# Performance work log

Hardware: AMD Instinct MI355X
Metric: run time of the kernel (lower is better)

The kernel has to match this reference:

```python
import jax, jax.numpy as jnp
import numpy as np

LOG_2PI = float(np.log(2.0 * np.pi))


def gaussian_log_density(samples, mean, log_squared_scale):
    inv_sigma = jnp.exp(-log_squared_scale)
    tmp = samples - mean
    return -0.5 * (tmp * tmp * inv_sigma + log_squared_scale + LOG_2PI)


def setup_inputs() -> dict:
    key = jax.random.key(0)
    k1, k2, k3, k4, k5 = jax.random.split(key, 5)
    B, L, D = 4096, 16, 512
    return {
        "data": jax.random.normal(k1, (B, D), dtype=jnp.float32),
        "reconstruction": jax.random.normal(k2, (B, D), dtype=jnp.float32),
        "z": jax.random.normal(k3, (B, L), dtype=jnp.float32),
        "z_mean": jax.random.normal(k4, (B, L), dtype=jnp.float32),
        "z_log_var": jax.random.normal(k5, (B, L), dtype=jnp.float32),
    }


def reference(data, reconstruction, z, z_mean, z_log_var):
    # reconstruction loss: mean over batch of per-sample MAE (mean over feature axis)
    recon_loss = jnp.mean(jnp.abs(data - reconstruction))

    # KL penalty: mean over batch of 0.5 * sum over latents
    summand = jnp.square(z_mean) + jnp.exp(z_log_var) - z_log_var - 1.0
    kl_loss = jnp.mean(0.5 * jnp.sum(summand, axis=1))

    # total correlation: pairwise gaussian log-density [B, B, L]
    log_qz_prob = gaussian_log_density(
        z[:, None, :], z_mean[None, :, :], z_log_var[None, :, :]
    )
    # log prod_l q(z_l): logsumexp over batch axis 1 per latent, then sum over latents
    log_qz_product = jnp.sum(jax.nn.logsumexp(log_qz_prob, axis=1), axis=1)
    # log q(z): sum over latents first, then logsumexp over batch axis
    log_qz = jax.nn.logsumexp(jnp.sum(log_qz_prob, axis=2), axis=1)
    tc_loss = jnp.mean(log_qz - log_qz_product)

    total_loss = recon_loss + kl_loss + tc_loss
    return total_loss
```

## Files before the change

kernel.cpp:

```cpp
#include <hip/hip_runtime.h>
#include <hip/hip_fp16.h>
#include <math.h>

#define BB 4096
#define LL 16
#define DD 512

#define NPTS   1024
#define XMIN   -6.0f
#define XRANGE 12.0f

#define LOG2E_F  1.4426950408889634f
#define LN2_F    0.6931471805599453f
#define LOG2PI_F 1.8378770664093453f

#define OFFC     22.942540f
#define SCALE23  8388608.0f
#define BIASF    126.94269504f

#if __has_builtin(__builtin_amdgcn_exp2f)
#define EXP2(x) __builtin_amdgcn_exp2f(x)
#else
#define EXP2(x) exp2f(x)
#endif
#if __has_builtin(__builtin_amdgcn_logf)
#define LOG2(x) __builtin_amdgcn_logf(x)
#else
#define LOG2(x) log2f(x)
#endif

typedef float f32x2 __attribute__((ext_vector_type(2)));

#define CJ_F   0
#define CT_F   147456
#define RP_F   344064
#define KLP_F  346112
#define TP_F   346368
#define TAB_F  870656
#define JP_F   887040

__device__ __forceinline__ float block_reduce(float v) {
  __shared__ float sm[4];
  __syncthreads();
#pragma unroll
  for (int off = 32; off; off >>= 1) v += __shfl_xor(v, off);
  if ((threadIdx.x & 63) == 0) sm[threadIdx.x >> 6] = v;
  __syncthreads();
  if (threadIdx.x == 0) v = (sm[0] + sm[1]) + (sm[2] + sm[3]);
  return v;
}

__global__ __launch_bounds__(256) void prep_recon_kernel(
    const float4* __restrict__ data4, const float4* __restrict__ recon4,
    const float* __restrict__ zm, const float* __restrict__ zlv,
    float* __restrict__ cj, float* __restrict__ ct,
    float* __restrict__ rp, float* __restrict__ klp,
    float* __restrict__ out) {
  const int tid = threadIdx.x;
  const int b = blockIdx.x;

  if (b == 1024 && tid == 0) out[0] = 0.0f;

  {
    const int n4 = (BB * DD) / 4;
    int stride = gridDim.x * 256;
    float s = 0.0f;
    for (int k = b * 256 + tid; k < n4; k += stride) {
      float4 a = data4[k];
      float4 r = recon4[k];
      s += (fabsf(a.x - r.x) + fabsf(a.y - r.y)) +
           (fabsf(a.z - r.z) + fabsf(a.w - r.w));
    }
    float t = block_reduce(s);
    if (tid == 0) rp[b] = t * (1.0f / (float)(BB * DD));
  }

  if (b < 256) {
    const float S = 1024.0f / 65535.0f;
    int idx = b * 256 + tid;
    int j = idx >> 4;
    int l = idx & 15;
    float m = zm[idx];
    float lv = zlv[idx];
    float inv = EXP2(-lv * LOG2E_F);
    float a = -0.5f * LOG2E_F * inv;
    float c2 = -0.5f * LOG2E_F * (lv + LOG2PI_F);
    float braw = -2.0f * a * m;
    float craw = fmaf(a, m * m, c2);

    cj[j * 36 + l]      = a * S;
    cj[j * 36 + 16 + l] = braw * S;
    float cs = (craw + OFFC) * S;
    cs += __shfl_xor(cs, 1); cs += __shfl_xor(cs, 2);
    cs += __shfl_xor(cs, 4); cs += __shfl_xor(cs, 8);
    if (l == 0) cj[j * 36 + 32] = cs;

    ct[(0 * 16 + l) * 4096 + j] = a;
    ct[(1 * 16 + l) * 4096 + j] = braw;
    ct[(2 * 16 + l) * 4096 + j] = craw;

    float kls = m * m + EXP2(lv * LOG2E_F) - lv - 1.0f;
    float s = block_reduce(kls);
    if (tid == 0) klp[b] = s * (0.5f / (float)BB);
  }
}

__global__ __launch_bounds__(256) void table_build(
    const float* __restrict__ ct, float* __restrict__ tpart) {
  __shared__ float la[128], lb[128], lc[128];
  const int tid = threadIdx.x;
  const int jc = blockIdx.x;
  const int l  = blockIdx.y;
  const int j0 = jc * 128;
  if (tid < 128) {
    la[tid] = ct[(0 * 16 + l) * 4096 + j0 + tid];
    lb[tid] = ct[(1 * 16 + l) * 4096 + j0 + tid];
    lc[tid] = ct[(2 * 16 + l) * 4096 + j0 + tid];
  }
  const float H = XRANGE / (float)(NPTS - 1);
  float x[4], acc[4];
#pragma unroll
  for (int k = 0; k < 4; ++k) {
    x[k] = XMIN + (float)(k * 256 + tid) * H;
    acc[k] = 0.0f;
  }
  __syncthreads();
#pragma unroll 2
  for (int j = 0; j < 128; ++j) {
    float a = la[j], b = lb[j], c = lc[j];
#pragma unroll
    for (int k = 0; k < 4; ++k) {
      float lp = fmaf(fmaf(a, x[k], b), x[k], c);
      acc[k] += EXP2(lp);
    }
  }
  float* o = tpart + ((size_t)jc * 16 + l) * NPTS;
#pragma unroll
  for (int k = 0; k < 4; ++k) o[k * 256 + tid] = acc[k];
}

__global__ __launch_bounds__(256) void table_reduce(
    const float* __restrict__ tpart, float* __restrict__ table) {
  const int e = blockIdx.x * 256 + threadIdx.x;
  float s = 0.0f;
#pragma unroll 4
  for (int jc = 0; jc < 32; ++jc) s += tpart[(size_t)jc * (16 * NPTS) + e];
  table[e] = s;
}

template <int CHUNK, int R>
__global__ __launch_bounds__(256, 2) void tc_joint(
    const float* __restrict__ z, const float* __restrict__ cj,
    float* __restrict__ jp) {
  __shared__ float lcj[CHUNK * 36];
  const int tid = threadIdx.x;
  const int i0 = blockIdx.x * (256 * R) + tid;
  const int j0 = blockIdx.y * CHUNK;
  const float JMUL = 65535.0f * 8192.0f;
  const float JK   = -SCALE23 * (16.0f * OFFC - BIASF);

  {
    const float4* g4 = (const float4*)(cj + (size_t)j0 * 36);
    float4* l4 = (float4*)lcj;
    for (int t = tid; t < (CHUNK * 36) / 4; t += 256) l4[t] = g4[t];
  }

  f32x2 zv[R][8];
#pragma unroll
  for (int r = 0; r < R; ++r) {
    const float4* zp = (const float4*)(z + (size_t)(i0 + 256 * r) * 16);
#pragma unroll
    for (int q = 0; q < 4; ++q) {
      float4 v = zp[q];
      zv[r][2 * q]     = (f32x2){v.x, v.y};
      zv[r][2 * q + 1] = (f32x2){v.z, v.w};
    }
  }
#pragma unroll
  for (int r = 0; r < R; ++r)
#pragma unroll
    for (int p = 0; p < 8; ++p) asm volatile("" : "+v"(zv[r][p]));

  float accJ[R];
#pragma unroll
  for (int r = 0; r < R; ++r) accJ[r] = 0.0f;

  __syncthreads();

#pragma unroll 2
  for (int j = 0; j < CHUNK; ++j) {
    const float* cp = lcj + j * 36;
    f32x2 A[8], Bv[8];
#pragma unroll
    for (int t = 0; t < 4; ++t) {
      *(float4*)&A[2 * t]  = *(const float4*)(cp + 4 * t);
      *(float4*)&Bv[2 * t] = *(const float4*)(cp + 16 + 4 * t);
    }
    float Cs = cp[32];
#pragma unroll
    for (int r = 0; r < R; ++r) {
      f32x2 acc = (f32x2){0.0f, 0.0f};
#pragma unroll
      for (int p = 0; p < 8; ++p) {
        f32x2 t2;
        asm("v_pk_fma_f32 %0, %1, %2, %3"
            : "=v"(t2) : "v"(A[p]), "v"(zv[r][p]), "v"(Bv[p]));
        asm("v_pk_fma_f32 %0, %1, %2, %0"
            : "+v"(acc) : "v"(t2), "v"(zv[r][p]));
      }
      float js = (acc.x + acc.y) + Cs;
      float w = fmaf(js, JMUL, JK);
      unsigned u;
      asm("v_cvt_u32_f32 %0, %1" : "=v"(u) : "v"(w));
      accJ[r] += __uint_as_float(u);
    }
  }

#pragma unroll
  for (int r = 0; r < R; ++r)
    jp[(size_t)blockIdx.y * BB + (size_t)(i0 + 256 * r)] = accJ[r];
}

__global__ __launch_bounds__(256) void final_kernel(
    const float* __restrict__ z, const float* __restrict__ jp,
    const float* __restrict__ table, const float* __restrict__ rp,
    const float* __restrict__ klp, float* __restrict__ out, int nc) {
  __shared__ float ltab[16 * NPTS];
  const int tid = threadIdx.x;
  const int i = blockIdx.x * 256 + tid;

  for (int t = tid; t < 16 * NPTS; t += 256) ltab[t] = table[t];

  float s0 = 0.0f, s1 = 0.0f, s2 = 0.0f, s3 = 0.0f;
  for (int c = 0; c < nc; c += 4) {
    s0 += jp[(size_t)(c + 0) * BB + i];
    s1 += jp[(size_t)(c + 1) * BB + i];
    s2 += jp[(size_t)(c + 2) * BB + i];
    s3 += jp[(size_t)(c + 3) * BB + i];
  }
  float lg = LOG2((s0 + s1) + (s2 + s3));

  __syncthreads();

  const float4* zp = (const float4*)(z + (size_t)i * 16);
  const float SC = (float)(NPTS - 1) / XRANGE;
#pragma unroll
  for (int q = 0; q < 4; ++q) {
    float4 v = zp[q];
    float xs[4] = {v.x, v.y, v.z, v.w};
#pragma unroll
    for (int k = 0; k < 4; ++k) {
      int l = 4 * q + k;
      float t = (xs[k] - XMIN) * SC;
      t = fminf(fmaxf(t, 0.0f), (float)(NPTS - 2) + 0.999f);
      int g = (int)t;
      float f = t - (float)g;
      float m0 = ltab[l * NPTS + g];
      float m1 = ltab[l * NPTS + g + 1];
      lg -= LOG2(fmaf(f, m1 - m0, m0));
    }
  }

  float tval = lg * (LN2_F / (float)BB);
  if (blockIdx.x == 0) {
#pragma unroll
    for (int q = 0; q < 8; ++q) tval += rp[tid + 256 * q];
    tval += klp[tid];
  }

  __syncthreads();
#pragma unroll
  for (int off = 32; off; off >>= 1) tval += __shfl_xor(tval, off);
  if ((tid & 63) == 0) ltab[tid >> 6] = tval;
  __syncthreads();
  if (tid == 0) atomicAdd(out, (ltab[0] + ltab[1]) + (ltab[2] + ltab[3]));
}

extern "C" void kernel_launch(void* const* d_in, const int* in_sizes, int n_in,
                              void* d_out, int out_size, void* d_ws, size_t ws_size,
                              hipStream_t stream) {
  const float* data  = (const float*)d_in[0];
  const float* recon = (const float*)d_in[1];
  const float* z     = (const float*)d_in[2];
  const float* zm    = (const float*)d_in[3];
  const float* zlv   = (const float*)d_in[4];
  float* out = (float*)d_out;
  float* ws  = (float*)d_ws;

  const int nc = 128;

  float* cj   = ws + CJ_F;
  float* ct   = ws + CT_F;
  float* rp   = ws + RP_F;
  float* klp  = ws + KLP_F;
  float* tp   = ws + TP_F;
  float* tab  = ws + TAB_F;
  float* jp   = ws + JP_F;

  hipLaunchKernelGGL(prep_recon_kernel, dim3(2048), dim3(256), 0, stream,
                     reinterpret_cast<const float4*>(data),
                     reinterpret_cast<const float4*>(recon),
                     zm, zlv, cj, ct, rp, klp, out);
  hipLaunchKernelGGL(table_build, dim3(32, 16), dim3(256), 0, stream,
                     ct, tp);
  hipLaunchKernelGGL(table_reduce, dim3((16 * NPTS) / 256), dim3(256), 0,
                     stream, tp, tab);
  hipLaunchKernelGGL((tc_joint<32, 4>), dim3(4, 128), dim3(256), 0, stream,
                     z, cj, jp);
  hipLaunchKernelGGL(final_kernel, dim3(BB / 256), dim3(256), 0, stream,
                     z, jp, tab, rp, klp, out, nc);
}
```

Measured before the change: 117.9 us.

## Fuse all stages into one cooperative persistent kernel with grid syncs

Merges the five launches (prep/recon, table build, table reduce, joint pairwise pass, final reduce) into one cooperative kernel of 512 blocks, separating stages with grid-wide syncs. It also transposes the joint partial-sum layout to row-major per sample so the final stage reads float4 contiguously, and runs the final lookups from global memory instead of staging the table in shared memory. This removes launch gaps and inter-kernel drains, but it adds grid-sync costs, uses fewer blocks for the recon pass and the final stage (16 blocks), and lowers parallelism in several phases.

```diff
diff --git a/kernel.cpp b/kernel.cpp
--- a/kernel.cpp
+++ b/kernel.cpp
@@ -1,6 +1,9 @@
 #include <hip/hip_runtime.h>
 #include <hip/hip_fp16.h>
+#include <hip/hip_cooperative_groups.h>
 #include <math.h>
+
+namespace cg = cooperative_groups;
 
 #define BB 4096
 #define LL 16
@@ -50,22 +53,23 @@
   return v;
 }
 
-__global__ __launch_bounds__(256) void prep_recon_kernel(
+__global__ __launch_bounds__(256, 2) void mega_kernel(
     const float4* __restrict__ data4, const float4* __restrict__ recon4,
     const float* __restrict__ zm, const float* __restrict__ zlv,
+    const float* __restrict__ z,
     float* __restrict__ cj, float* __restrict__ ct,
     float* __restrict__ rp, float* __restrict__ klp,
-    float* __restrict__ out) {
+    float* __restrict__ tp, float* __restrict__ tab,
+    float* __restrict__ jp, float* __restrict__ out) {
+  cg::grid_group grid = cg::this_grid();
   const int tid = threadIdx.x;
   const int b = blockIdx.x;
 
-  if (b == 1024 && tid == 0) out[0] = 0.0f;
-
+  if (b == 0 && tid == 0) out[0] = 0.0f;
   {
     const int n4 = (BB * DD) / 4;
-    int stride = gridDim.x * 256;
     float s = 0.0f;
-    for (int k = b * 256 + tid; k < n4; k += stride) {
+    for (int k = b * 256 + tid; k < n4; k += 512 * 256) {
       float4 a = data4[k];
       float4 r = recon4[k];
       s += (fabsf(a.x - r.x) + fabsf(a.y - r.y)) +
@@ -74,7 +78,6 @@
     float t = block_reduce(s);
     if (tid == 0) rp[b] = t * (1.0f / (float)(BB * DD));
   }
-
   if (b < 256) {
     const float S = 1024.0f / 65535.0f;
     int idx = b * 256 + tid;
@@ -103,210 +106,184 @@
     float s = block_reduce(kls);
     if (tid == 0) klp[b] = s * (0.5f / (float)BB);
   }
-}
-
-__global__ __launch_bounds__(256) void table_build(
-    const float* __restrict__ ct, float* __restrict__ tpart) {
-  __shared__ float la[128], lb[128], lc[128];
-  const int tid = threadIdx.x;
-  const int jc = blockIdx.x;
-  const int l  = blockIdx.y;
-  const int j0 = jc * 128;
-  if (tid < 128) {
-    la[tid] = ct[(0 * 16 + l) * 4096 + j0 + tid];
-    lb[tid] = ct[(1 * 16 + l) * 4096 + j0 + tid];
-    lc[tid] = ct[(2 * 16 + l) * 4096 + j0 + tid];
-  }
-  const float H = XRANGE / (float)(NPTS - 1);
-  float x[4], acc[4];
-#pragma unroll
-  for (int k = 0; k < 4; ++k) {
-    x[k] = XMIN + (float)(k * 256 + tid) * H;
-    acc[k] = 0.0f;
-  }
-  __syncthreads();
+  grid.sync();
+
+  {
+    __shared__ float la[128], lb[128], lc[128];
+    const int jc = b >> 4;
+    const int l  = b & 15;
+    const int j0 = jc * 128;
+    if (tid < 128) {
+      la[tid] = ct[(0 * 16 + l) * 4096 + j0 + tid];
+      lb[tid] = ct[(1 * 16 + l) * 4096 + j0 + tid];
+      lc[tid] = ct[(2 * 16 + l) * 4096 + j0 + tid];
+    }
+    const float H = XRANGE / (float)(NPTS - 1);
+    float x[4], acc[4];
+#pragma unroll
+    for (int k = 0; k < 4; ++k) {
+      x[k] = XMIN + (float)(k * 256 + tid) * H;
+      acc[k] = 0.0f;
+    }
+    __syncthreads();
 #pragma unroll 2
-  for (int j = 0; j < 128; ++j) {
-    float a = la[j], b = lb[j], c = lc[j];
-#pragma unroll
-    for (int k = 0; k < 4; ++k) {
-      float lp = fmaf(fmaf(a, x[k], b), x[k], c);
-      acc[k] += EXP2(lp);
-    }
-  }
-  float* o = tpart + ((size_t)jc * 16 + l) * NPTS;
-#pragma unroll
-  for (int k = 0; k < 4; ++k) o[k * 256 + tid] = acc[k];
-}
-
-__global__ __launch_bounds__(256) void table_reduce(
-    const float* __restrict__ tpart, float* __restrict__ table) {
-  const int e = blockIdx.x * 256 + threadIdx.x;
-  float s = 0.0f;
+    for (int j = 0; j < 128; ++j) {
+      float a = la[j], bb = lb[j], c = lc[j];
+#pragma unroll
+      for (int k = 0; k < 4; ++k) {
+        float lp = fmaf(fmaf(a, x[k], bb), x[k], c);
+        acc[k] += EXP2(lp);
+      }
+    }
+    float* o = tp + ((size_t)jc * 16 + l) * NPTS;
+#pragma unroll
+    for (int k = 0; k < 4; ++k) o[k * 256 + tid] = acc[k];
+  }
+  grid.sync();
+
+  if (b < 64) {
+    const int e = b * 256 + tid;
+    float s = 0.0f;
 #pragma unroll 4
-  for (int jc = 0; jc < 32; ++jc) s += tpart[(size_t)jc * (16 * NPTS) + e];
-  table[e] = s;
-}
-
-template <int CHUNK, int R>
-__global__ __launch_bounds__(256, 2) void tc_joint(
-    const float* __restrict__ z, const float* __restrict__ cj,
-    float* __restrict__ jp) {
-  __shared__ float lcj[CHUNK * 36];
-  const int tid = threadIdx.x;
-  const int i0 = blockIdx.x * (256 * R) + tid;
-  const int j0 = blockIdx.y * CHUNK;
-  const float JMUL = 65535.0f * 8192.0f;
-  const float JK   = -SCALE23 * (16.0f * OFFC - BIASF);
+    for (int jc = 0; jc < 32; ++jc) s += tp[(size_t)jc * (16 * NPTS) + e];
+    tab[e] = s;
+  }
 
   {
-    const float4* g4 = (const float4*)(cj + (size_t)j0 * 36);
-    float4* l4 = (float4*)lcj;
-    for (int t = tid; t < (CHUNK * 36) / 4; t += 256) l4[t] = g4[t];
-  }
-
-  f32x2 zv[R][8];
-#pragma unroll
-  for (int r = 0; r < R; ++r) {
-    const float4* zp = (const float4*)(z + (size_t)(i0 + 256 * r) * 16);
+    __shared__ float lcj[32 * 36];
+    const int bx = b & 3;
+    const int by = b >> 2;
+    const int i0 = bx * 1024 + tid;
+    const int j0 = by * 32;
+    const float JMUL = 65535.0f * 8192.0f;
+    const float JK   = -SCALE23 * (16.0f * OFFC - BIASF);
+
+    {
+      const float4* g4 = (const float4*)(cj + (size_t)j0 * 36);
+      float4* l4 = (float4*)lcj;
+      for (int t = tid; t < (32 * 36) / 4; t += 256) l4[t] = g4[t];
+    }
+
+    f32x2 zv[4][8];
+#pragma unroll
+    for (int r = 0; r < 4; ++r) {
+      const float4* zp = (const float4*)(z + (size_t)(i0 + 256 * r) * 16);
+#pragma unroll
+      for (int q = 0; q < 4; ++q) {
+        float4 v = zp[q];
+        zv[r][2 * q]     = (f32x2){v.x, v.y};
+        zv[r][2 * q + 1] = (f32x2){v.z, v.w};
+      }
+    }
+#pragma unroll
+    for (int r = 0; r < 4; ++r)
+#pragma unroll
+      for (int p = 0; p < 8; ++p) asm volatile("" : "+v"(zv[r][p]));
+
+    float accJ[4] = {0.0f, 0.0f, 0.0f, 0.0f};
+
+    __syncthreads();
+
+#pragma unroll 2
+    for (int j = 0; j < 32; ++j) {
+      const float* cp = lcj + j * 36;
+      f32x2 A[8], Bv[8];
+#pragma unroll
+      for (int t = 0; t < 4; ++t) {
+        *(float4*)&A[2 * t]  = *(const float4*)(cp + 4 * t);
+        *(float4*)&Bv[2 * t] = *(const float4*)(cp + 16 + 4 * t);
+      }
+      float Cs = cp[32];
+#pragma unroll
+      for (int r = 0; r < 4; ++r) {
+        f32x2 acc = (f32x2){0.0f, 0.0f};
+#pragma unroll
+        for (int p = 0; p < 8; ++p) {
+          f32x2 t2;
+          asm("v_pk_fma_f32 %0, %1, %2, %3"
+              : "=v"(t2) : "v"(A[p]), "v"(zv[r][p]), "v"(Bv[p]));
+          asm("v_pk_fma_f32 %0, %1, %2, %0"
+              : "+v"(acc) : "v"(t2), "v"(zv[r][p]));
+        }
+        float js = (acc.x + acc.y) + Cs;
+        float w = fmaf(js, JMUL, JK);
+        unsigned u;
+        asm("v_cvt_u32_f32 %0, %1" : "=v"(u) : "v"(w));
+        accJ[r] += __uint_as_float(u);
+      }
+    }
+
+#pragma unroll
+    for (int r = 0; r < 4; ++r)
+      jp[(size_t)(i0 + 256 * r) * 128 + by] = accJ[r];
+  }
+  grid.sync();
+
+  if (b < 16) {
+    const int i = b * 256 + tid;
+
+    float s0 = 0.0f, s1 = 0.0f, s2 = 0.0f, s3 = 0.0f;
+    const float4* jr = (const float4*)(jp + (size_t)i * 128);
+#pragma unroll 8
+    for (int c = 0; c < 32; ++c) {
+      float4 v = jr[c];
+      s0 += v.x; s1 += v.y; s2 += v.z; s3 += v.w;
+    }
+    float lg = LOG2((s0 + s1) + (s2 + s3));
+
+    const float4* zp = (const float4*)(z + (size_t)i * 16);
+    const float SC = (float)(NPTS - 1) / XRANGE;
 #pragma unroll
     for (int q = 0; q < 4; ++q) {
       float4 v = zp[q];
-      zv[r][2 * q]     = (f32x2){v.x, v.y};
-      zv[r][2 * q + 1] = (f32x2){v.z, v.w};
-    }
-  }
-#pragma unroll
-  for (int r = 0; r < R; ++r)
-#pragma unroll
-    for (int p = 0; p < 8; ++p) asm volatile("" : "+v"(zv[r][p]));
-
-  float accJ[R];
-#pragma unroll
-  for (int r = 0; r < R; ++r) accJ[r] = 0.0f;
-
-  __syncthreads();
-
-#pragma unroll 2
-  for (int j = 0; j < CHUNK; ++j) {
-    const float* cp = lcj + j * 36;
-    f32x2 A[8], Bv[8];
-#pragma unroll
-    for (int t = 0; t < 4; ++t) {
-      *(float4*)&A[2 * t]  = *(const float4*)(cp + 4 * t);
-      *(float4*)&Bv[2 * t] = *(const float4*)(cp + 16 + 4 * t);
-    }
-    float Cs = cp[32];
-#pragma unroll
-    for (int r = 0; r < R; ++r) {
-      f32x2 acc = (f32x2){0.0f, 0.0f};
-#pragma unroll
-      for (int p = 0; p < 8; ++p) {
-        f32x2 t2;
-        asm("v_pk_fma_f32 %0, %1, %2, %3"
-            : "=v"(t2) : "v"(A[p]), "v"(zv[r][p]), "v"(Bv[p]));
-        asm("v_pk_fma_f32 %0, %1, %2, %0"
-            : "+v"(acc) : "v"(t2), "v"(zv[r][p]));
-      }
-      float js = (acc.x + acc.y) + Cs;
-      float w = fmaf(js, JMUL, JK);
-      unsigned u;
-      asm("v_cvt_u32_f32 %0, %1" : "=v"(u) : "v"(w));
-      accJ[r] += __uint_as_float(u);
-    }
-  }
-
-#pragma unroll
-  for (int r = 0; r < R; ++r)
-    jp[(size_t)blockIdx.y * BB + (size_t)(i0 + 256 * r)] = accJ[r];
-}
-
-__global__ __launch_bounds__(256) void final_kernel(
-    const float* __restrict__ z, const float* __restrict__ jp,
-    const float* __restrict__ table, const float* __restrict__ rp,
-    const float* __restrict__ klp, float* __restrict__ out, int nc) {
-  __shared__ float ltab[16 * NPTS];
-  const int tid = threadIdx.x;
-  const int i = blockIdx.x * 256 + tid;
-
-  for (int t = tid; t < 16 * NPTS; t += 256) ltab[t] = table[t];
-
-  float s0 = 0.0f, s1 = 0.0f, s2 = 0.0f, s3 = 0.0f;
-  for (int c = 0; c < nc; c += 4) {
-    s0 += jp[(size_t)(c + 0) * BB + i];
-    s1 += jp[(size_t)(c + 1) * BB + i];
-    s2 += jp[(size_t)(c + 2) * BB + i];
-    s3 += jp[(size_t)(c + 3) * BB + i];
-  }
-  float lg = LOG2((s0 + s1) + (s2 + s3));
-
-  __syncthreads();
-
-  const float4* zp = (const float4*)(z + (size_t)i * 16);
-  const float SC = (float)(NPTS - 1) / XRANGE;
-#pragma unroll
-  for (int q = 0; q < 4; ++q) {
-    float4 v = zp[q];
-    float xs[4] = {v.x, v.y, v.z, v.w};
-#pragma unroll
-    for (int k = 0; k < 4; ++k) {
-      int l = 4 * q + k;
-      float t = (xs[k] - XMIN) * SC;
-      t = fminf(fmaxf(t, 0.0f), (float)(NPTS - 2) + 0.999f);
-      int g = (int)t;
-      float f = t - (float)g;
-      float m0 = ltab[l * NPTS + g];
-      float m1 = ltab[l * NPTS + g + 1];
-      lg -= LOG2(fmaf(f, m1 - m0, m0));
-    }
-  }
-
-  float tval = lg * (LN2_F / (float)BB);
-  if (blockIdx.x == 0) {
-#pragma unroll
-    for (int q = 0; q < 8; ++q) tval += rp[tid + 256 * q];
-    tval += klp[tid];
-  }
-
-  __syncthreads();
-#pragma unroll
-  for (int off = 32; off; off >>= 1) tval += __shfl_xor(tval, off);
-  if ((tid & 63) == 0) ltab[tid >> 6] = tval;
-  __syncthreads();
-  if (tid == 0) atomicAdd(out, (ltab[0] + ltab[1]) + (ltab[2] + ltab[3]));
+      float xs[4] = {v.x, v.y, v.z, v.w};
+#pragma unroll
+      for (int k = 0; k < 4; ++k) {
+        int l = 4 * q + k;
+        float t = (xs[k] - XMIN) * SC;
+        t = fminf(fmaxf(t, 0.0f), (float)(NPTS - 2) + 0.999f);
+        int g = (int)t;
+        float f = t - (float)g;
+        float m0 = tab[l * NPTS + g];
+        float m1 = tab[l * NPTS + g + 1];
+        lg -= LOG2(fmaf(f, m1 - m0, m0));
+      }
+    }
+
+    float tval = lg * (LN2_F / (float)BB);
+    if (b == 0) {
+      tval += rp[tid] + rp[tid + 256];
+      tval += klp[tid];
+    }
+    float s = block_reduce(tval);
+    if (tid == 0) atomicAdd(out, s);
+  }
 }
 
 extern "C" void kernel_launch(void* const* d_in, const int* in_sizes, int n_in,
                               void* d_out, int out_size, void* d_ws, size_t ws_size,
                               hipStream_t stream) {
-  const float* data  = (const float*)d_in[0];
-  const float* recon = (const float*)d_in[1];
-  const float* z     = (const float*)d_in[2];
-  const float* zm    = (const float*)d_in[3];
-  const float* zlv   = (const float*)d_in[4];
+  const float4* data4  = (const float4*)d_in[0];
+  const float4* recon4 = (const float4*)d_in[1];
+  const float* z       = (const float*)d_in[2];
+  const float* zm      = (const float*)d_in[3];
+  const float* zlv     = (const float*)d_in[4];
   float* out = (float*)d_out;
   float* ws  = (float*)d_ws;
 
-  const int nc = 128;
-
-  float* cj   = ws + CJ_F;
-  float* ct   = ws + CT_F;
-  float* rp   = ws + RP_F;
-  float* klp  = ws + KLP_F;
-  float* tp   = ws + TP_F;
-  float* tab  = ws + TAB_F;
-  float* jp   = ws + JP_F;
-
-  hipLaunchKernelGGL(prep_recon_kernel, dim3(2048), dim3(256), 0, stream,
-                     reinterpret_cast<const float4*>(data),
-                     reinterpret_cast<const float4*>(recon),
-                     zm, zlv, cj, ct, rp, klp, out);
-  hipLaunchKernelGGL(table_build, dim3(32, 16), dim3(256), 0, stream,
-                     ct, tp);
-  hipLaunchKernelGGL(table_reduce, dim3((16 * NPTS) / 256), dim3(256), 0,
-                     stream, tp, tab);
-  hipLaunchKernelGGL((tc_joint<32, 4>), dim3(4, 128), dim3(256), 0, stream,
-                     z, cj, jp);
-  hipLaunchKernelGGL(final_kernel, dim3(BB / 256), dim3(256), 0, stream,
-                     z, jp, tab, rp, klp, out, nc);
+  float* cj  = ws + CJ_F;
+  float* ct  = ws + CT_F;
+  float* rp  = ws + RP_F;
+  float* klp = ws + KLP_F;
+  float* tp  = ws + TP_F;
+  float* tab = ws + TAB_F;
+  float* jp  = ws + JP_F;
+
+  void* args[] = {
+      (void*)&data4, (void*)&recon4, (void*)&zm, (void*)&zlv, (void*)&z,
+      (void*)&cj, (void*)&ct, (void*)&rp, (void*)&klp,
+      (void*)&tp, (void*)&tab, (void*)&jp, (void*)&out};
+
+  hipLaunchCooperativeKernel((const void*)mega_kernel, dim3(512), dim3(256),
+                             args, 0, stream);
 }
```

After: 305.8 us. 159% more time.
